# Kernel tuning notes

Hardware: AMD Instinct MI355X
Metric: run time of the kernel (lower is better)

Reference implementation:

```python
import jax, jax.numpy as jnp
import numpy as np

B, T, D, H, STRIDE, MLP = 2, 2048, 1024, 16, 8, 4096
HD = D // H
EPS = 1e-5


def _ln(x, g, b):
    m = x.mean(-1, keepdims=True)
    v = x.var(-1, keepdims=True)
    return (x - m) * jax.lax.rsqrt(v + EPS) * g + b


def setup_inputs() -> dict:
    key = jax.random.key(0)
    ks = jax.random.split(key, 6)
    s = lambda k, shape: (jax.random.normal(k, shape, jnp.float32) * 0.02)
    return {
        "x": jax.random.normal(ks[0], (B, T, D), jnp.float32),
        "w_in": s(ks[1], (3 * D, D)),   # torch in_proj_weight
        "b_in": jnp.zeros((3 * D,), jnp.float32),
        "w_out": s(ks[2], (D, D)),      # attn out_proj
        "b_out": jnp.zeros((D,), jnp.float32),
        "w1": s(ks[3], (MLP, D)),       # mlp first Linear (torch layout [out,in])
        "b1": jnp.zeros((MLP,), jnp.float32),
        "w2": s(ks[4], (D, MLP)),       # mlp second Linear
        "b2": jnp.zeros((D,), jnp.float32),
        "ln1_g": jnp.ones((D,), jnp.float32),
        "ln1_b": jnp.zeros((D,), jnp.float32),
        "ln2_g": jnp.ones((D,), jnp.float32),
        "ln2_b": jnp.zeros((D,), jnp.float32),
    }


def reference(x, w_in, b_in, w_out, b_out, w1, b1, w2, b2,
              ln1_g, ln1_b, ln2_g, ln2_b):
    Bs, Ts, Ds = x.shape
    xn = _ln(x, ln1_g, ln1_b)
    # fused qkv projection (torch Linear: y = x @ W.T + b)
    qkv = xn @ w_in.T + b_in                              # [B,T,3D]
    q, k, v = jnp.split(qkv, 3, axis=-1)
    to_heads = lambda t: t.reshape(Bs, Ts, H, HD).transpose(0, 2, 1, 3)
    q, k, v = to_heads(q), to_heads(k), to_heads(v)       # [B,H,T,hd]
    scores = jnp.einsum("bhqd,bhkd->bhqk", q, k) / jnp.sqrt(jnp.float32(HD))
    # mask: rows at multiples of STRIDE attend everywhere; others only to self
    idx = jnp.arange(Ts)
    allowed = ((idx % STRIDE) == 0)[:, None] | (idx[:, None] == idx[None, :])
    scores = jnp.where(allowed, scores, -jnp.inf)
    attn = jax.nn.softmax(scores, axis=-1)
    o = jnp.einsum("bhqk,bhkd->bhqd", attn, v)            # [B,H,T,hd]
    o = o.transpose(0, 2, 1, 3).reshape(Bs, Ts, Ds)
    o = o @ w_out.T + b_out
    x = x + o
    xn = _ln(x, ln2_g, ln2_b)
    h = jax.nn.gelu(xn @ w1.T + b1, approximate=False)    # torch nn.GELU default = exact
    x = x + (h @ w2.T + b2)
    return x
```

## Files before the change

kernel.cpp:

```cpp
#include <hip/hip_runtime.h>

#define D_ 1024
#define T_ 2048
#define B_ 2
#define H_ 16
#define MLP_ 4096
#define NTOK (B_*T_)
#define QG 256
#define L2E 1.44269504088896340736f

typedef float f32x4 __attribute__((ext_vector_type(4)));
typedef __bf16 bf16x8 __attribute__((ext_vector_type(8)));

__device__ __forceinline__ unsigned short f2bf(float f) {
  unsigned int u = __float_as_uint(f);
  u += 0x7fff + ((u >> 16) & 1);
  return (unsigned short)(u >> 16);
}

__device__ __forceinline__ float wave_sum(float v) {
  for (int o = 32; o > 0; o >>= 1) v += __shfl_down(v, o, 64);
  return v;
}

__device__ __forceinline__ void gload16(const unsigned short* g, unsigned short* l) {
  __builtin_amdgcn_global_load_lds(
      (const __attribute__((address_space(1))) void*)g,
      (__attribute__((address_space(3))) void*)l, 16, 0, 0);
}

__device__ __forceinline__ unsigned ldsoff(const void* p) {
  return (unsigned)(size_t)(const __attribute__((address_space(3))) void*)p;
}

__device__ __forceinline__ void agload16(const unsigned short* g, unsigned m0v) {
  unsigned su = __builtin_amdgcn_readfirstlane(m0v);
  asm volatile("s_mov_b32 m0, %0\n\t"
               "global_load_lds_dwordx4 %1, off"
               :: "s"(su), "v"(g) : "memory");
}

#define N4_WIN  786432
#define N4_WOUT 262144
#define N4_W1   1048576
#define N4_W2   1048576
#define NCASTB  12288
__global__ void castln_kernel(const float* __restrict__ w_in,
                              const float* __restrict__ w_out,
                              const float* __restrict__ w1,
                              const float* __restrict__ w2,
                              unsigned short* __restrict__ o_in,
                              unsigned short* __restrict__ o_out,
                              unsigned short* __restrict__ o1,
                              unsigned short* __restrict__ o2,
                              const float* __restrict__ x,
                              const float* __restrict__ g,
                              const float* __restrict__ b,
                              unsigned short* __restrict__ xn) {
  int blk = blockIdx.x;
  int tid = threadIdx.x;
  if (blk < NTOK) {
    int wave = tid >> 6, lane = tid & 63;
    float4 v = ((const float4*)(x + (size_t)blk * D_))[tid];
    float s  = v.x + v.y + v.z + v.w;
    float s2 = v.x*v.x + v.y*v.y + v.z*v.z + v.w*v.w;
    s = wave_sum(s); s2 = wave_sum(s2);
    __shared__ float r1[4], r2[4];
    if (lane == 0) { r1[wave] = s; r2[wave] = s2; }
    __syncthreads();
    float ts  = r1[0] + r1[1] + r1[2] + r1[3];
    float ts2 = r2[0] + r2[1] + r2[2] + r2[3];
    float mean = ts * (1.0f / D_);
    float var  = ts2 * (1.0f / D_) - mean * mean;
    float rs = rsqrtf(var + 1e-5f);
    float4 gv = ((const float4*)g)[tid];
    float4 bv = ((const float4*)b)[tid];
    ushort4 o;
    o.x = f2bf((v.x - mean) * rs * gv.x + bv.x);
    o.y = f2bf((v.y - mean) * rs * gv.y + bv.y);
    o.z = f2bf((v.z - mean) * rs * gv.z + bv.z);
    o.w = f2bf((v.w - mean) * rs * gv.w + bv.w);
    ((ushort4*)(xn + (size_t)blk * D_))[tid] = o;
  } else {
    int i = (blk - NTOK) * 256 + tid;
    const float* src; unsigned short* dst; int j = i;
    if (i < N4_WIN) { src = w_in; dst = o_in; }
    else if ((j -= N4_WIN) < N4_WOUT) { src = w_out; dst = o_out; }
    else if ((j -= N4_WOUT) < N4_W1) { src = w1; dst = o1; }
    else { j -= N4_W1; src = w2; dst = o2; }
    float4 v = ((const float4*)src)[j];
    ushort4 o;
    o.x = f2bf(v.x); o.y = f2bf(v.y); o.z = f2bf(v.z); o.w = f2bf(v.w);
    ((ushort4*)dst)[j] = o;
  }
}

__global__ void ln_kernel(const float* __restrict__ x, const float* __restrict__ g,
                          const float* __restrict__ b, unsigned short* __restrict__ out) {
  int row = blockIdx.x;
  int tid = threadIdx.x;
  int wave = tid >> 6, lane = tid & 63;
  float4 v = ((const float4*)(x + (size_t)row * D_))[tid];
  float s  = v.x + v.y + v.z + v.w;
  float s2 = v.x*v.x + v.y*v.y + v.z*v.z + v.w*v.w;
  s = wave_sum(s); s2 = wave_sum(s2);
  __shared__ float r1[4], r2[4];
  if (lane == 0) { r1[wave] = s; r2[wave] = s2; }
  __syncthreads();
  float ts  = r1[0] + r1[1] + r1[2] + r1[3];
  float ts2 = r2[0] + r2[1] + r2[2] + r2[3];
  float mean = ts * (1.0f / D_);
  float var  = ts2 * (1.0f / D_) - mean * mean;
  float rs = rsqrtf(var + 1e-5f);
  float4 gv = ((const float4*)g)[tid];
  float4 bv = ((const float4*)b)[tid];
  ushort4 o;
  o.x = f2bf((v.x - mean) * rs * gv.x + bv.x);
  o.y = f2bf((v.y - mean) * rs * gv.y + bv.y);
  o.z = f2bf((v.z - mean) * rs * gv.z + bv.z);
  o.w = f2bf((v.w - mean) * rs * gv.w + bv.w);
  ((ushort4*)(out + (size_t)row * D_))[tid] = o;
}

__global__ __launch_bounds__(256)
void gemm64p_kernel(const unsigned short* __restrict__ A, int LDA,
                    const unsigned short* __restrict__ Bm, int LDB,
                    float* __restrict__ C,
                    const float* __restrict__ bias,
                    const float* __restrict__ xres,
                    int K, int nx) {
  __shared__ __align__(16) unsigned short As[2 * 4096];
  __shared__ __align__(16) unsigned short Bs[2 * 8192];
  const int tid = threadIdx.x;
  const int lane = tid & 63, wave = tid >> 6;
  const int wm = (wave >> 1) * 32, wn = (wave & 1) * 64;
  const int fr = lane & 15, q = lane >> 4;
  const int f0 = ((q)     ^ (fr & 7)) << 3;
  const int f1 = ((4 + q) ^ (fr & 7)) << 3;

  const int nwg = gridDim.x;
  const int bid = blockIdx.x;
  const int l = (bid & 7) * (nwg >> 3) + (bid >> 3);
  const int bx = l % nx, by = l / nx;
  const int m0 = by * 64, n0 = bx * 128;

  const unsigned short* aS[2];
  const unsigned short* bS[4];
#pragma unroll
  for (int p = 0; p < 2; ++p) {
    int ls = p * 256 + tid;
    int r = ls >> 3;
    int cg = (ls & 7) ^ (r & 7);
    aS[p] = A + (size_t)(m0 + r) * LDA + cg * 8;
  }
#pragma unroll
  for (int p = 0; p < 4; ++p) {
    int ls = p * 256 + tid;
    int r = ls >> 3;
    int cg = (ls & 7) ^ (r & 7);
    bS[p] = Bm + (size_t)(n0 + r) * LDB + cg * 8;
  }
  const int NT = K >> 6;

  const unsigned aW = ldsoff(As) + wave * 1024;
  const unsigned bW = ldsoff(Bs) + wave * 1024;

#pragma unroll
  for (int p = 0; p < 2; ++p) agload16(aS[p], aW + p * 4096);
#pragma unroll
  for (int p = 0; p < 4; ++p) agload16(bS[p], bW + p * 4096);
#pragma unroll
  for (int p = 0; p < 2; ++p) agload16(aS[p] + 64, aW + 8192 + p * 4096);
#pragma unroll
  for (int p = 0; p < 4; ++p) agload16(bS[p] + 64, bW + 16384 + p * 4096);
  asm volatile("s_waitcnt vmcnt(6)");
  __builtin_amdgcn_sched_barrier(0);
  __builtin_amdgcn_s_barrier();

  f32x4 acc[2][4] = {};
  for (int t = 0; t < NT; ++t) {
    const int cbA = (t & 1) << 12;
    const int cbB = (t & 1) << 13;
    const unsigned cbAB = (t & 1) << 13;
    const unsigned cbBB = (t & 1) << 14;
    const unsigned short* Ab = As + cbA;
    const unsigned short* Bb = Bs + cbB;
    const int ko2 = (t + 2) << 6;
    {
      bf16x8 af[2], bfr[4];
#pragma unroll
      for (int i = 0; i < 2; ++i) af[i]  = *(const bf16x8*)&Ab[(wm + i * 16 + fr) * 64 + f0];
#pragma unroll
      for (int j = 0; j < 4; ++j) bfr[j] = *(const bf16x8*)&Bb[(wn + j * 16 + fr) * 64 + f0];
#pragma unroll
      for (int i = 0; i < 2; ++i)
#pragma unroll
        for (int j = 0; j < 4; ++j)
          acc[i][j] = __builtin_amdgcn_mfma_f32_16x16x32_bf16(af[i], bfr[j], acc[i][j], 0, 0, 0);
    }
    {
      bf16x8 af[2], bfr[4];
#pragma unroll
      for (int i = 0; i < 2; ++i) af[i]  = *(const bf16x8*)&Ab[(wm + i * 16 + fr) * 64 + f1];
#pragma unroll
      for (int j = 0; j < 4; ++j) bfr[j] = *(const bf16x8*)&Bb[(wn + j * 16 + fr) * 64 + f1];
#pragma unroll
      for (int i = 0; i < 2; ++i)
#pragma unroll
        for (int j = 0; j < 4; ++j)
          acc[i][j] = __builtin_amdgcn_mfma_f32_16x16x32_bf16(af[i], bfr[j], acc[i][j], 0, 0, 0);
    }
    __builtin_amdgcn_s_barrier();
    if (t + 2 < NT) {
#pragma unroll
      for (int p = 0; p < 2; ++p) agload16(aS[p] + ko2, aW + cbAB + p * 4096);
#pragma unroll
      for (int p = 0; p < 4; ++p) agload16(bS[p] + ko2, bW + cbBB + p * 4096);
    }
    if (t + 1 < NT) {
      if (t + 2 < NT) asm volatile("s_waitcnt vmcnt(6)");
      else            asm volatile("s_waitcnt vmcnt(0)");
      __builtin_amdgcn_sched_barrier(0);
    }
    __builtin_amdgcn_s_barrier();
  }

  const int col = lane & 15, rbase = (lane >> 4) * 4;
#pragma unroll
  for (int i = 0; i < 2; ++i) {
#pragma unroll
    for (int j = 0; j < 4; ++j) {
      int gn = n0 + wn + j * 16 + col;
      int gmb = m0 + wm + i * 16 + rbase;
      float bv = bias[gn];
#pragma unroll
      for (int r = 0; r < 4; ++r) {
        int gm = gmb + r;
        size_t idx = (size_t)gm * D_ + gn;
        C[idx] = acc[i][j][r] + bv + xres[idx];
      }
    }
  }
}

template<int EPI>
__global__ __launch_bounds__(512)
void gemm256a_kernel(const unsigned short* __restrict__ A, int LDA,
                     const unsigned short* __restrict__ Bm, int LDB,
                     void* __restrict__ Cv, size_t sC, int LDC,
                     const float* __restrict__ bias,
                     int K, int nx) {
  __shared__ __align__(16) unsigned short As[2 * 16384];
  __shared__ __align__(16) unsigned short Bs[2 * 16384];
  const int tid = threadIdx.x;
  const int lane = tid & 63, w = tid >> 6;
  const int wm = w >> 2, wn = w & 3;
  const int fr = lane & 15, q = lane >> 4, xr = fr & 7;

  const int nwg = gridDim.x;
  const int bid = blockIdx.x;
  const int l = (bid & 7) * (nwg >> 3) + (bid >> 3);
  const int bx = l % nx, by = l / nx;
  const int m0 = by * 256, n0 = bx * 256;
  const int kOff = blockIdx.z * K;

  const unsigned short* aS[4];
  const unsigned short* bS[4];
#pragma unroll
  for (int s = 0; s < 4; ++s) {
    int ls = s * 512 + tid;
    int r = ls >> 3;
    int cg = (ls & 7) ^ (r & 7);
    aS[s] = A  + (size_t)(m0 + r) * LDA + kOff + cg * 8;
    bS[s] = Bm + (size_t)(n0 + r) * LDB + kOff + cg * 8;
  }
  const int NT = K >> 6;

  const unsigned asb = ldsoff(As), bsb = ldsoff(Bs);
  const unsigned aW = asb + w * 1024, bW = bsb + w * 1024;

#pragma unroll
  for (int s = 0; s < 4; ++s) {
    agload16(aS[s], aW + s * 8192);
    agload16(bS[s], bW + s * 8192);
  }
#pragma unroll
  for (int s = 0; s < 4; ++s) {
    agload16(aS[s] + 64, aW + 32768 + s * 8192);
    agload16(bS[s] + 64, bW + 32768 + s * 8192);
  }
  asm volatile("s_waitcnt vmcnt(8)");
  __builtin_amdgcn_sched_barrier(0);
  __builtin_amdgcn_s_barrier();

  const int aOff = ((wm * 128 + fr) << 7) + ((q ^ xr) << 4);
  const int bOff = ((wn * 64 + fr) << 7) + ((q ^ xr) << 4);

  f32x4 acc[8][4] = {};

  for (int t = 0; t < NT; ++t) {
    const int cb = (t & 1) << 15;
    const char* Ab = (const char*)As + cb;
    const char* Bb = (const char*)Bs + cb;
    const unsigned aWc = aW + cb, bWc = bW + cb;
    const int ko2 = (t + 2) << 6;
    bf16x8 af[2][4], bfr[2][4];

#pragma unroll
    for (int i = 0; i < 4; ++i) {
      af[0][i] = *(const bf16x8*)(Ab + aOff + i * 2048);
      af[1][i] = *(const bf16x8*)(Ab + (aOff ^ 64) + i * 2048);
    }
#pragma unroll
    for (int j = 0; j < 2; ++j) {
      bfr[0][j] = *(const bf16x8*)(Bb + bOff + j * 2048);
      bfr[1][j] = *(const bf16x8*)(Bb + (bOff ^ 64) + j * 2048);
    }
    __builtin_amdgcn_s_barrier();
    __builtin_amdgcn_s_setprio(1);
#pragma unroll
    for (int i = 0; i < 4; ++i)
#pragma unroll
      for (int j = 0; j < 2; ++j) {
        acc[i][j] = __builtin_amdgcn_mfma_f32_16x16x32_bf16(af[0][i], bfr[0][j], acc[i][j], 0, 0, 0);
        acc[i][j] = __builtin_amdgcn_mfma_f32_16x16x32_bf16(af[1][i], bfr[1][j], acc[i][j], 0, 0, 0);
      }
    __builtin_amdgcn_s_setprio(0);
    __builtin_amdgcn_s_barrier();

#pragma unroll
    for (int j = 2; j < 4; ++j) {
      bfr[0][j] = *(const bf16x8*)(Bb + bOff + j * 2048);
      bfr[1][j] = *(const bf16x8*)(Bb + (bOff ^ 64) + j * 2048);
    }
    if (t + 2 < NT) {
      agload16(aS[0] + ko2, aWc);
      agload16(aS[2] + ko2, aWc + 16384);
    }
    __builtin_amdgcn_s_barrier();
    __builtin_amdgcn_s_setprio(1);
#pragma unroll
    for (int i = 0; i < 4; ++i)
#pragma unroll
      for (int j = 0; j < 2; ++j) {
        acc[i][2 + j] = __builtin_amdgcn_mfma_f32_16x16x32_bf16(af[0][i], bfr[0][2 + j], acc[i][2 + j], 0, 0, 0);
        acc[i][2 + j] = __builtin_amdgcn_mfma_f32_16x16x32_bf16(af[1][i], bfr[1][2 + j], acc[i][2 + j], 0, 0, 0);
      }
    __builtin_amdgcn_s_setprio(0);
    __builtin_amdgcn_s_barrier();

#pragma unroll
    for (int i = 0; i < 4; ++i) {
      af[0][i] = *(const bf16x8*)(Ab + (aOff + 8192) + i * 2048);
      af[1][i] = *(const bf16x8*)(Ab + ((aOff + 8192) ^ 64) + i * 2048);
    }
    if (t + 2 < NT) {
      agload16(bS[0] + ko2, bWc);
      agload16(bS[1] + ko2, bWc + 8192);
      agload16(bS[2] + ko2, bWc + 16384);
      agload16(bS[3] + ko2, bWc + 24576);
    }
    __builtin_amdgcn_s_barrier();
    __builtin_amdgcn_s_setprio(1);
#pragma unroll
    for (int i = 0; i < 4; ++i)
#pragma unroll
      for (int j = 0; j < 2; ++j) {
        acc[4 + i][j] = __builtin_amdgcn_mfma_f32_16x16x32_bf16(af[0][i], bfr[0][j], acc[4 + i][j], 0, 0, 0);
        acc[4 + i][j] = __builtin_amdgcn_mfma_f32_16x16x32_bf16(af[1][i], bfr[1][j], acc[4 + i][j], 0, 0, 0);
      }
    __builtin_amdgcn_s_setprio(0);
    __builtin_amdgcn_s_barrier();

    if (t + 2 < NT) {
      agload16(aS[1] + ko2, aWc + 8192);
      agload16(aS[3] + ko2, aWc + 24576);
    }
    if (t + 1 < NT) {
      if (t + 2 < NT) asm volatile("s_waitcnt vmcnt(8)");
      else            asm volatile("s_waitcnt vmcnt(0)");
      __builtin_amdgcn_sched_barrier(0);
    }
    __builtin_amdgcn_s_barrier();
    __builtin_amdgcn_s_setprio(1);
#pragma unroll
    for (int i = 0; i < 4; ++i)
#pragma unroll
      for (int j = 0; j < 2; ++j) {
        acc[4 + i][2 + j] = __builtin_amdgcn_mfma_f32_16x16x32_bf16(af[0][i], bfr[0][2 + j], acc[4 + i][2 + j], 0, 0, 0);
        acc[4 + i][2 + j] = __builtin_amdgcn_mfma_f32_16x16x32_bf16(af[1][i], bfr[1][2 + j], acc[4 + i][2 + j], 0, 0, 0);
      }
    __builtin_amdgcn_s_setprio(0);
    __builtin_amdgcn_s_barrier();
  }

  const int col = lane & 15, rbase = (lane >> 4) * 4;
  const int gm0 = m0 + wm * 128 + rbase;
  const int gn0 = n0 + wn * 64 + col;
#pragma unroll
  for (int mi = 0; mi < 8; ++mi) {
#pragma unroll
    for (int j = 0; j < 4; ++j) {
      int gn = gn0 + j * 16;
      float bv = (EPI == 2) ? bias[gn] : 0.0f;
#pragma unroll
      for (int r = 0; r < 4; ++r) {
        int gm = gm0 + mi * 16 + r;
        float v = acc[mi][j][r] + bv;
        if (EPI == 2) {
          float u = v * (1.5957691216f + 0.0713548162f * v * v);
          float gl = v / (1.0f + exp2f(-L2E * u));
          ((unsigned short*)Cv)[(size_t)gm * LDC + gn] = f2bf(gl);
        } else {
          ((float*)Cv)[(size_t)blockIdx.z * sC + (size_t)gm * LDC + gn] = v;
        }
      }
    }
  }
}

template<int EPI>
__global__ __launch_bounds__(512)
void gemm256b_kernel(const unsigned short* __restrict__ A, int LDA,
                     const unsigned short* __restrict__ Bm, int LDB,
                     unsigned short* __restrict__ Cv, int LDC,
                     const float* __restrict__ bias,
                     unsigned short* __restrict__ aux1,
                     unsigned short* __restrict__ aux2,
                     int K, int nx) {
  __shared__ __align__(16) unsigned short As[2 * 4096];
  __shared__ __align__(16) unsigned short Bs[2 * 8192];
  const int tid = threadIdx.x;
  const int lane = tid & 63, wv = tid >> 6;
  const int wm = (wv >> 2) * 64, wn = (wv & 3) * 64;
  const int fr = lane & 15, q = lane >> 4;

  const int nwg = gridDim.x;
  const int bid = blockIdx.x;
  const int l = (bid & 7) * (nwg >> 3) + (bid >> 3);
  const int bx = l % nx, by = l / nx;
  const int m0 = by * 128, n0 = bx * 256;

  const int rA = tid >> 2, sA = tid & 3;
  const int cA = sA ^ ((rA >> 1) & 3);
  const unsigned short* aSrc = A  + (size_t)(m0 + rA) * LDA + cA * 8;
  const unsigned short* bSrc0 = Bm + (size_t)(n0 + rA) * LDB + cA * 8;
  const unsigned short* bSrc1 = Bm + (size_t)(n0 + 128 + rA) * LDB + cA * 8;
  const int NT = K >> 5;

  const unsigned aWb = ldsoff(As) + wv * 1024;
  const unsigned bWb = ldsoff(Bs) + wv * 1024;

  agload16(aSrc, aWb);
  agload16(bSrc0, bWb);
  agload16(bSrc1, bWb + 8192);
  agload16(aSrc + 32, aWb + 8192);
  agload16(bSrc0 + 32, bWb + 16384);
  agload16(bSrc1 + 32, bWb + 24576);
  asm volatile("s_waitcnt vmcnt(3)");
  __builtin_amdgcn_sched_barrier(0);
  __builtin_amdgcn_s_barrier();

  f32x4 acc[4][4] = {};
  for (int t = 0; t < NT; ++t) {
    const unsigned cbA = (t & 1) ? 8192u : 0u;
    const unsigned cbB = (t & 1) ? 16384u : 0u;
    const char* Ab = (const char*)As + cbA;
    const char* Bb = (const char*)Bs + cbB;
    const int ko2 = (t + 2) << 5;
    bf16x8 af[4], bfr[4];
#pragma unroll
    for (int i = 0; i < 4; ++i) {
      int ra = wm + i * 16 + fr;
      af[i] = *(const bf16x8*)(Ab + ra * 64 + ((q ^ ((ra >> 1) & 3)) << 4));
    }
#pragma unroll
    for (int j = 0; j < 4; ++j) {
      int rb = wn + j * 16 + fr;
      bfr[j] = *(const bf16x8*)(Bb + rb * 64 + ((q ^ ((rb >> 1) & 3)) << 4));
    }
#pragma unroll
    for (int i = 0; i < 4; ++i)
#pragma unroll
      for (int j = 0; j < 4; ++j)
        acc[i][j] = __builtin_amdgcn_mfma_f32_16x16x32_bf16(af[i], bfr[j], acc[i][j], 0, 0, 0);
    __builtin_amdgcn_s_barrier();
    if (t + 2 < NT) {
      agload16(aSrc + ko2, aWb + cbA);
      agload16(bSrc0 + ko2, bWb + cbB);
      agload16(bSrc1 + ko2, bWb + cbB + 8192);
    }
    if (t + 1 < NT) {
      if (t + 2 < NT) asm volatile("s_waitcnt vmcnt(3)");
      else            asm volatile("s_waitcnt vmcnt(0)");
      __builtin_amdgcn_sched_barrier(0);
    }
    __builtin_amdgcn_s_barrier();
  }

  const int col = lane & 15, rbase = (lane >> 4) * 4;
#pragma unroll
  for (int i = 0; i < 4; ++i) {
#pragma unroll
    for (int j = 0; j < 4; ++j) {
      int gn = n0 + wn + j * 16 + col;
      int gmb = m0 + wm + i * 16 + rbase;
      float bv = bias[gn];
#pragma unroll
      for (int r = 0; r < 4; ++r) {
        int gm = gmb + r;
        float v = acc[i][j][r] + bv;
        if (EPI == 2) {
          float u = v * (1.5957691216f + 0.0713548162f * v * v);
          float gl = v / (1.0f + exp2f(-L2E * u));
          Cv[(size_t)gm * LDC + gn] = f2bf(gl);
        } else {
          int sec = gn >> 10;
          int hh = (gn >> 6) & (H_ - 1);
          int dd = gn & 63;
          int t = gm & (T_ - 1);
          int b = gm >> 11;
          unsigned short bf = f2bf(v);
          if (sec == 0) {
            if (!(t & 7))
              aux1[(((size_t)(b * H_ + hh)) * QG + (t >> 3)) * 64 + dd] = bf;
          } else if (sec == 1) {
            aux2[(((size_t)(b * H_ + hh)) * T_ + t) * 64 + dd] = bf;
          } else {
            Cv[(size_t)gm * D_ + (gn - 2 * D_)] = bf;
          }
        }
      }
    }
  }
}

__global__ void vtrans_kernel(const unsigned short* __restrict__ vcomp,
                              unsigned short* __restrict__ Vt) {
  int blk = blockIdx.x;
  int tchunk = blk & 31;
  int bh = blk >> 5;
  int h = bh & (H_ - 1), b = bh >> 4;
  int t0 = tchunk * 64;
  __shared__ unsigned short ls[64][66];
  int tid = threadIdx.x;
#pragma unroll
  for (int it = 0; it < 16; ++it) {
    int linear = it * 256 + tid;
    int d = linear & 63, tl = linear >> 6;
    ls[d][tl] = vcomp[((size_t)(b * T_ + t0 + tl)) * D_ + h * 64 + d];
  }
  __syncthreads();
#pragma unroll
  for (int it = 0; it < 16; ++it) {
    int linear = it * 256 + tid;
    int tl = linear & 63, d = linear >> 6;
    Vt[((size_t)(bh * 64 + d)) * T_ + t0 + tl] = ls[d][tl];
  }
}

__global__ __launch_bounds__(256)
void flash_kernel(const unsigned short* __restrict__ Qg,
                  const unsigned short* __restrict__ Kh,
                  const unsigned short* __restrict__ Vt,
                  float* __restrict__ Opart,
                  float* __restrict__ ml) {
  const int kc = blockIdx.x, qt = blockIdx.y, bh = blockIdx.z;
  const int tid = threadIdx.x;
  const int lane = tid & 63, w = tid >> 6;
  const int fr = lane & 15, quad = lane >> 4;

  __shared__ __align__(16) unsigned short Qs[64 * 64];
  __shared__ __align__(16) unsigned short Ks[128 * 64];
  __shared__ __align__(16) unsigned short Vs[64 * 128];
  __shared__ __align__(16) unsigned short Ps[4 * 16 * 128];

  const unsigned short* Qbase = Qg + ((size_t)bh * 256 + qt * 64) * 64;
#pragma unroll
  for (int p = 0; p < 2; ++p) {
    int linear = p * 256 + tid;
    int r = linear >> 3, c = linear & 7;
    gload16(Qbase + r * 64 + (c ^ (r & 7)) * 8, &Qs[linear * 8]);
  }

  float m_run[4], l_run[4];
  f32x4 O[4] = {};
#pragma unroll
  for (int r = 0; r < 4; ++r) { m_run[r] = -3.0e38f; l_run[r] = 0.f; }

  const unsigned short* Kc = Kh + ((size_t)bh * T_ + kc * 512) * 64;
  const unsigned short* Vc = Vt + (size_t)bh * 64 * T_ + kc * 512;
  unsigned short* Pw = &Ps[w * 2048];
  const int arow = w * 16 + fr;

  for (int kt = 0; kt < 4; ++kt) {
    __syncthreads();
#pragma unroll
    for (int p = 0; p < 4; ++p) {
      int linear = p * 256 + tid;
      int r = linear >> 3, c = linear & 7;
      gload16(Kc + (size_t)(kt * 128 + r) * 64 + (c ^ (r & 7)) * 8, &Ks[linear * 8]);
    }
#pragma unroll
    for (int p = 0; p < 4; ++p) {
      int linear = p * 256 + tid;
      int r = linear >> 4, c = linear & 15;
      gload16(Vc + (size_t)r * T_ + kt * 128 + (c ^ (r & 7)) * 8, &Vs[linear * 8]);
    }
    __syncthreads();

    f32x4 s[8] = {};
    bf16x8 aq[2];
#pragma unroll
    for (int ks = 0; ks < 2; ++ks)
      aq[ks] = *(const bf16x8*)&Qs[arow * 64 + ((ks * 4 + quad) ^ (fr & 7)) * 8];
#pragma unroll
    for (int nf = 0; nf < 8; ++nf) {
      int krow = nf * 16 + fr;
#pragma unroll
      for (int ks = 0; ks < 2; ++ks) {
        bf16x8 bk = *(const bf16x8*)&Ks[krow * 64 + ((ks * 4 + quad) ^ (fr & 7)) * 8];
        s[nf] = __builtin_amdgcn_mfma_f32_16x16x32_bf16(aq[ks], bk, s[nf], 0, 0, 0);
      }
    }
    float alpha[4], rowsum[4];
#pragma unroll
    for (int r = 0; r < 4; ++r) {
      float mt = -3.0e38f;
#pragma unroll
      for (int nf = 0; nf < 8; ++nf) { s[nf][r] *= 0.125f; mt = fmaxf(mt, s[nf][r]); }
#pragma unroll
      for (int x = 1; x < 16; x <<= 1) mt = fmaxf(mt, __shfl_xor(mt, x, 64));
      float mn = fmaxf(m_run[r], mt);
      alpha[r] = exp2f((m_run[r] - mn) * L2E);
      m_run[r] = mn;
      rowsum[r] = 0.f;
    }
#pragma unroll
    for (int nf = 0; nf < 8; ++nf)
#pragma unroll
      for (int r = 0; r < 4; ++r) {
        float p = exp2f((s[nf][r] - m_run[r]) * L2E);
        s[nf][r] = p; rowsum[r] += p;
      }
#pragma unroll
    for (int r = 0; r < 4; ++r) {
#pragma unroll
      for (int x = 1; x < 16; x <<= 1) rowsum[r] += __shfl_xor(rowsum[r], x, 64);
      l_run[r] = l_run[r] * alpha[r] + rowsum[r];
    }
#pragma unroll
    for (int nf = 0; nf < 8; ++nf)
#pragma unroll
      for (int r = 0; r < 4; ++r) {
        int m = quad * 4 + r;
        int c = nf * 2 + (fr >> 3);
        Pw[m * 128 + ((c ^ (m & 7)) * 8) + (fr & 7)] = f2bf(s[nf][r]);
      }
#pragma unroll
    for (int nf2 = 0; nf2 < 4; ++nf2)
#pragma unroll
      for (int r = 0; r < 4; ++r) O[nf2][r] *= alpha[r];
#pragma unroll
    for (int ks2 = 0; ks2 < 4; ++ks2) {
      bf16x8 ap = *(const bf16x8*)&Pw[fr * 128 + (((ks2 * 4 + quad) ^ (fr & 7)) * 8)];
#pragma unroll
      for (int nf2 = 0; nf2 < 4; ++nf2) {
        int vrow = nf2 * 16 + fr;
        bf16x8 bv = *(const bf16x8*)&Vs[vrow * 128 + (((ks2 * 4 + quad) ^ (fr & 7)) * 8)];
        O[nf2] = __builtin_amdgcn_mfma_f32_16x16x32_bf16(ap, bv, O[nf2], 0, 0, 0);
      }
    }
  }

  int qbase = qt * 64 + w * 16;
  float* Ob = Opart + (((size_t)bh * 4 + kc) * 256 + qbase) * 64;
#pragma unroll
  for (int nf2 = 0; nf2 < 4; ++nf2)
#pragma unroll
    for (int r = 0; r < 4; ++r)
      Ob[(size_t)(quad * 4 + r) * 64 + nf2 * 16 + fr] = O[nf2][r];
  if (fr == 0) {
#pragma unroll
    for (int r = 0; r < 4; ++r) {
      size_t mi = ((((size_t)bh * 4 + kc) * 256) + qbase + quad * 4 + r) * 2;
      ml[mi] = m_run[r]; ml[mi + 1] = l_run[r];
    }
  }
}

__global__ void combine_kernel(const float* __restrict__ Opart,
                               const float* __restrict__ ml,
                               unsigned short* __restrict__ vcomp) {
  int idx = blockIdx.x * 256 + threadIdx.x;
  int c = idx & (D_ - 1);
  int qi = (idx >> 10) & (QG - 1);
  int b = idx >> 18;
  int h = c >> 6, d = c & 63;
  int bh = b * H_ + h;
  float m[4], l[4];
  float M = -3.0e38f;
#pragma unroll
  for (int ch = 0; ch < 4; ++ch) {
    size_t r = ((size_t)bh * 4 + ch) * 256 + qi;
    m[ch] = ml[r * 2]; l[ch] = ml[r * 2 + 1];
    M = fmaxf(M, m[ch]);
  }
  float osum = 0.f, lsum = 0.f;
#pragma unroll
  for (int ch = 0; ch < 4; ++ch) {
    size_t r = ((size_t)bh * 4 + ch) * 256 + qi;
    float wgt = exp2f((m[ch] - M) * L2E);
    osum += wgt * Opart[r * 64 + d];
    lsum += wgt * l[ch];
  }
  vcomp[((size_t)(b * T_ + qi * 8)) * D_ + c] = f2bf(osum / lsum);
}

extern "C" void kernel_launch(void* const* d_in, const int* in_sizes, int n_in,
                              void* d_out, int out_size, void* d_ws, size_t ws_size,
                              hipStream_t stream) {
  const float* x     = (const float*)d_in[0];
  const float* w_in  = (const float*)d_in[1];
  const float* b_in  = (const float*)d_in[2];
  const float* w_out = (const float*)d_in[3];
  const float* b_out = (const float*)d_in[4];
  const float* w1    = (const float*)d_in[5];
  const float* b1    = (const float*)d_in[6];
  const float* w2    = (const float*)d_in[7];
  const float* b2    = (const float*)d_in[8];
  const float* ln1_g = (const float*)d_in[9];
  const float* ln1_b = (const float*)d_in[10];
  const float* ln2_g = (const float*)d_in[11];
  const float* ln2_b = (const float*)d_in[12];
  float* out = (float*)d_out;

  char* ws = (char*)d_ws;
  size_t off = 0;
  auto alloc = [&](size_t bytes) -> void* {
    void* p = ws + off;
    off += (bytes + 255) & ~(size_t)255;
    return p;
  };
  unsigned short* w_inb = (unsigned short*)alloc((size_t)3 * D_ * D_ * 2);
  unsigned short* w_outb= (unsigned short*)alloc((size_t)D_ * D_ * 2);
  unsigned short* w1b   = (unsigned short*)alloc((size_t)MLP_ * D_ * 2);
  unsigned short* w2b   = (unsigned short*)alloc((size_t)D_ * MLP_ * 2);
  unsigned short* vcomp = (unsigned short*)alloc((size_t)NTOK * D_ * 2);
  float*          x1    = (float*)         alloc((size_t)NTOK * D_ * 4);
  unsigned short* xn2   = (unsigned short*)alloc((size_t)NTOK * D_ * 2);
  unsigned short* h     = (unsigned short*)alloc((size_t)NTOK * MLP_ * 2);
  char* U = (char*)alloc((size_t)40 * 1024 * 1024);
  unsigned short* xn    = (unsigned short*)U;
  unsigned short* Qg    = (unsigned short*)(U + 8388608);
  unsigned short* Kh    = (unsigned short*)(U + 12582912);
  unsigned short* Vt    = (unsigned short*)(U + 20971520);
  float*          Opart = (float*)         (U + 29360128);
  float*          mlbuf = (float*)         (U + 37748736);

  castln_kernel<<<NTOK + NCASTB, 256, 0, stream>>>(
      w_in, w_out, w1, w2, w_inb, w_outb, w1b, w2b, x, ln1_g, ln1_b, xn);

  gemm256b_kernel<8><<<dim3(384, 1, 1), 512, 0, stream>>>(
      xn, D_, w_inb, D_, vcomp, 3 * D_, b_in, Qg, Kh, 1024, 12);

  vtrans_kernel<<<1024, 256, 0, stream>>>(vcomp, Vt);

  flash_kernel<<<dim3(4, 4, 32), 256, 0, stream>>>(Qg, Kh, Vt, Opart, mlbuf);

  combine_kernel<<<2048, 256, 0, stream>>>(Opart, mlbuf, vcomp);

  gemm64p_kernel<<<dim3(512, 1, 1), 256, 0, stream>>>(
      vcomp, D_, w_outb, D_, x1, b_out, x, 1024, 8);

  ln_kernel<<<NTOK, 256, 0, stream>>>(x1, ln2_g, ln2_b, xn2);

  gemm256a_kernel<2><<<dim3(256, 1, 1), 512, 0, stream>>>(
      xn2, D_, w1b, D_, h, 0, MLP_, b1, 1024, 16);

  gemm64p_kernel<<<dim3(512, 1, 1), 256, 0, stream>>>(
      h, MLP_, w2b, MLP_, out, b2, x1, 4096, 8);
}
```

Measured before the change: 294.0 us.

## Compute Q projection only for strided query rows in separate gathered GEMM

The fused QKV GEMM is split into two launches. One computes K and V for all tokens using the 64x128 tile kernel. The other gathers only every eighth token row (the global query rows) and computes Q for those alone, writing straight into the grouped Q buffer. This avoids computing seven eighths of the Q projection that was previously thrown away in the epilogue, at the cost of an extra launch and a small 64-block Q GEMM that underfills the device.

```diff
diff --git a/kernel.cpp b/kernel.cpp
--- a/kernel.cpp
+++ b/kernel.cpp
@@ -122,12 +122,15 @@
   ((ushort4*)(out + (size_t)row * D_))[tid] = o;
 }
 
+template<int EPI, int GA>
 __global__ __launch_bounds__(256)
-void gemm64p_kernel(const unsigned short* __restrict__ A, int LDA,
+void gemm64t_kernel(const unsigned short* __restrict__ A, int LDA,
                     const unsigned short* __restrict__ Bm, int LDB,
-                    float* __restrict__ C,
+                    void* __restrict__ Cv,
                     const float* __restrict__ bias,
                     const float* __restrict__ xres,
+                    unsigned short* __restrict__ aux1,
+                    unsigned short* __restrict__ aux2,
                     int K, int nx) {
   __shared__ __align__(16) unsigned short As[2 * 4096];
   __shared__ __align__(16) unsigned short Bs[2 * 8192];
@@ -151,7 +154,9 @@
     int ls = p * 256 + tid;
     int r = ls >> 3;
     int cg = (ls & 7) ^ (r & 7);
-    aS[p] = A + (size_t)(m0 + r) * LDA + cg * 8;
+    int gr = m0 + r;
+    size_t arow = GA ? ((size_t)(gr >> 8) * T_ + (gr & 255) * 8) : (size_t)gr;
+    aS[p] = A + arow * LDA + cg * 8;
   }
 #pragma unroll
   for (int p = 0; p < 4; ++p) {
@@ -236,8 +241,27 @@
 #pragma unroll
       for (int r = 0; r < 4; ++r) {
         int gm = gmb + r;
-        size_t idx = (size_t)gm * D_ + gn;
-        C[idx] = acc[i][j][r] + bv + xres[idx];
+        float v = acc[i][j][r] + bv;
+        if (EPI == 0) {
+          size_t idx = (size_t)gm * D_ + gn;
+          ((float*)Cv)[idx] = v + xres[idx];
+        } else if (EPI == 9) {
+          int sec = gn >> 10;
+          int hh = (gn >> 6) & (H_ - 1);
+          int dd = gn & 63;
+          int t = gm & (T_ - 1);
+          int b = gm >> 11;
+          unsigned short bf = f2bf(v);
+          if (sec == 0) {
+            aux2[(((size_t)(b * H_ + hh)) * T_ + t) * 64 + dd] = bf;
+          } else {
+            ((unsigned short*)Cv)[(size_t)gm * D_ + (gn - D_)] = bf;
+          }
+        } else {
+          int b = gm >> 8, qi = gm & 255;
+          int hh = gn >> 6, dd = gn & 63;
+          aux1[(((size_t)(b * H_ + hh)) * QG + qi) * 64 + dd] = f2bf(v);
+        }
       }
     }
   }
@@ -413,122 +437,6 @@
           ((unsigned short*)Cv)[(size_t)gm * LDC + gn] = f2bf(gl);
         } else {
           ((float*)Cv)[(size_t)blockIdx.z * sC + (size_t)gm * LDC + gn] = v;
-        }
-      }
-    }
-  }
-}
-
-template<int EPI>
-__global__ __launch_bounds__(512)
-void gemm256b_kernel(const unsigned short* __restrict__ A, int LDA,
-                     const unsigned short* __restrict__ Bm, int LDB,
-                     unsigned short* __restrict__ Cv, int LDC,
-                     const float* __restrict__ bias,
-                     unsigned short* __restrict__ aux1,
-                     unsigned short* __restrict__ aux2,
-                     int K, int nx) {
-  __shared__ __align__(16) unsigned short As[2 * 4096];
-  __shared__ __align__(16) unsigned short Bs[2 * 8192];
-  const int tid = threadIdx.x;
-  const int lane = tid & 63, wv = tid >> 6;
-  const int wm = (wv >> 2) * 64, wn = (wv & 3) * 64;
-  const int fr = lane & 15, q = lane >> 4;
-
-  const int nwg = gridDim.x;
-  const int bid = blockIdx.x;
-  const int l = (bid & 7) * (nwg >> 3) + (bid >> 3);
-  const int bx = l % nx, by = l / nx;
-  const int m0 = by * 128, n0 = bx * 256;
-
-  const int rA = tid >> 2, sA = tid & 3;
-  const int cA = sA ^ ((rA >> 1) & 3);
-  const unsigned short* aSrc = A  + (size_t)(m0 + rA) * LDA + cA * 8;
-  const unsigned short* bSrc0 = Bm + (size_t)(n0 + rA) * LDB + cA * 8;
-  const unsigned short* bSrc1 = Bm + (size_t)(n0 + 128 + rA) * LDB + cA * 8;
-  const int NT = K >> 5;
-
-  const unsigned aWb = ldsoff(As) + wv * 1024;
-  const unsigned bWb = ldsoff(Bs) + wv * 1024;
-
-  agload16(aSrc, aWb);
-  agload16(bSrc0, bWb);
-  agload16(bSrc1, bWb + 8192);
-  agload16(aSrc + 32, aWb + 8192);
-  agload16(bSrc0 + 32, bWb + 16384);
-  agload16(bSrc1 + 32, bWb + 24576);
-  asm volatile("s_waitcnt vmcnt(3)");
-  __builtin_amdgcn_sched_barrier(0);
-  __builtin_amdgcn_s_barrier();
-
-  f32x4 acc[4][4] = {};
-  for (int t = 0; t < NT; ++t) {
-    const unsigned cbA = (t & 1) ? 8192u : 0u;
-    const unsigned cbB = (t & 1) ? 16384u : 0u;
-    const char* Ab = (const char*)As + cbA;
-    const char* Bb = (const char*)Bs + cbB;
-    const int ko2 = (t + 2) << 5;
-    bf16x8 af[4], bfr[4];
-#pragma unroll
-    for (int i = 0; i < 4; ++i) {
-      int ra = wm + i * 16 + fr;
-      af[i] = *(const bf16x8*)(Ab + ra * 64 + ((q ^ ((ra >> 1) & 3)) << 4));
-    }
-#pragma unroll
-    for (int j = 0; j < 4; ++j) {
-      int rb = wn + j * 16 + fr;
-      bfr[j] = *(const bf16x8*)(Bb + rb * 64 + ((q ^ ((rb >> 1) & 3)) << 4));
-    }
-#pragma unroll
-    for (int i = 0; i < 4; ++i)
-#pragma unroll
-      for (int j = 0; j < 4; ++j)
-        acc[i][j] = __builtin_amdgcn_mfma_f32_16x16x32_bf16(af[i], bfr[j], acc[i][j], 0, 0, 0);
-    __builtin_amdgcn_s_barrier();
-    if (t + 2 < NT) {
-      agload16(aSrc + ko2, aWb + cbA);
-      agload16(bSrc0 + ko2, bWb + cbB);
-      agload16(bSrc1 + ko2, bWb + cbB + 8192);
-    }
-    if (t + 1 < NT) {
-      if (t + 2 < NT) asm volatile("s_waitcnt vmcnt(3)");
-      else            asm volatile("s_waitcnt vmcnt(0)");
-      __builtin_amdgcn_sched_barrier(0);
-    }
-    __builtin_amdgcn_s_barrier();
-  }
-
-  const int col = lane & 15, rbase = (lane >> 4) * 4;
-#pragma unroll
-  for (int i = 0; i < 4; ++i) {
-#pragma unroll
-    for (int j = 0; j < 4; ++j) {
-      int gn = n0 + wn + j * 16 + col;
-      int gmb = m0 + wm + i * 16 + rbase;
-      float bv = bias[gn];
-#pragma unroll
-      for (int r = 0; r < 4; ++r) {
-        int gm = gmb + r;
-        float v = acc[i][j][r] + bv;
-        if (EPI == 2) {
-          float u = v * (1.5957691216f + 0.0713548162f * v * v);
-          float gl = v / (1.0f + exp2f(-L2E * u));
-          Cv[(size_t)gm * LDC + gn] = f2bf(gl);
-        } else {
-          int sec = gn >> 10;
-          int hh = (gn >> 6) & (H_ - 1);
-          int dd = gn & 63;
-          int t = gm & (T_ - 1);
-          int b = gm >> 11;
-          unsigned short bf = f2bf(v);
-          if (sec == 0) {
-            if (!(t & 7))
-              aux1[(((size_t)(b * H_ + hh)) * QG + (t >> 3)) * 64 + dd] = bf;
-          } else if (sec == 1) {
-            aux2[(((size_t)(b * H_ + hh)) * T_ + t) * 64 + dd] = bf;
-          } else {
-            Cv[(size_t)gm * D_ + (gn - 2 * D_)] = bf;
-          }
         }
       }
     }
@@ -761,8 +669,13 @@
   castln_kernel<<<NTOK + NCASTB, 256, 0, stream>>>(
       w_in, w_out, w1, w2, w_inb, w_outb, w1b, w2b, x, ln1_g, ln1_b, xn);
 
-  gemm256b_kernel<8><<<dim3(384, 1, 1), 512, 0, stream>>>(
-      xn, D_, w_inb, D_, vcomp, 3 * D_, b_in, Qg, Kh, 1024, 12);
+  gemm64t_kernel<9, 0><<<dim3(1024, 1, 1), 256, 0, stream>>>(
+      xn, D_, w_inb + (size_t)D_ * D_, D_, vcomp, b_in + D_, nullptr,
+      nullptr, Kh, 1024, 16);
+
+  gemm64t_kernel<10, 1><<<dim3(64, 1, 1), 256, 0, stream>>>(
+      xn, D_, w_inb, D_, nullptr, b_in, nullptr,
+      Qg, nullptr, 1024, 8);
 
   vtrans_kernel<<<1024, 256, 0, stream>>>(vcomp, Vt);
 
@@ -770,14 +683,14 @@
 
   combine_kernel<<<2048, 256, 0, stream>>>(Opart, mlbuf, vcomp);
 
-  gemm64p_kernel<<<dim3(512, 1, 1), 256, 0, stream>>>(
-      vcomp, D_, w_outb, D_, x1, b_out, x, 1024, 8);
+  gemm64t_kernel<0, 0><<<dim3(512, 1, 1), 256, 0, stream>>>(
+      vcomp, D_, w_outb, D_, x1, b_out, x, nullptr, nullptr, 1024, 8);
 
   ln_kernel<<<NTOK, 256, 0, stream>>>(x1, ln2_g, ln2_b, xn2);
 
   gemm256a_kernel<2><<<dim3(256, 1, 1), 512, 0, stream>>>(
       xn2, D_, w1b, D_, h, 0, MLP_, b1, 1024, 16);
 
-  gemm64p_kernel<<<dim3(512, 1, 1), 256, 0, stream>>>(
-      h, MLP_, w2b, MLP_, out, b2, x1, 4096, 8);
-}
+  gemm64t_kernel<0, 0><<<dim3(512, 1, 1), 256, 0, stream>>>(
+      h, MLP_, w2b, MLP_, out, b2, x1, nullptr, nullptr, 4096, 8);
+}
```

Measured after the change: 309.4 us. +5.2%, slower.
